# Performance work log

Measured on AMD Instinct MI355X. Metric: run time of the kernel, lower is better.

Reference implementation:

```python
import jax, jax.numpy as jnp
import numpy as np

B, T, C, H = 8, 1024, 768, 12  # GPT-2 small attention, block_size=1024

def setup_inputs() -> dict:
    key = jax.random.key(0)
    k0, k1, k2 = jax.random.split(key, 3)
    return {
        "x": jax.random.normal(k0, (1, B, T, C), jnp.float32) * 0.02,
        "w_attn": jax.random.normal(k1, (C, 3 * C), jnp.float32) * 0.02,
        "b_attn": jnp.zeros((3 * C,), jnp.float32),
        "w_proj": jax.random.normal(k2, (C, C), jnp.float32) * 0.02,
        "b_proj": jnp.zeros((C,), jnp.float32),
    }

def reference(x, w_attn, b_attn, w_proj, b_proj):
    _, b, t, c = x.shape
    d = c // H  # head dim
    xb = x[0]  # [B,T,C]
    qkv = xb @ w_attn + b_attn  # [B,T,3C]
    q, k, v = jnp.split(qkv, 3, axis=-1)
    def to_heads(u):
        return u.reshape(b, t, H, d).transpose(0, 2, 1, 3)  # [B,H,T,D]
    q, k, v = to_heads(q), to_heads(k), to_heads(v)
    scale = 1.0 / jnp.sqrt(jnp.asarray(d, q.dtype))
    att = jnp.einsum('bhqd,bhkd->bhqk', q, k) * scale  # [B,H,T,T]
    causal = jnp.tril(jnp.ones((t, t), bool))
    att = jnp.where(causal, att, -jnp.inf)
    att = jax.nn.softmax(att, axis=-1)
    y = jnp.einsum('bhqk,bhkd->bhqd', att, v)  # [B,H,T,D]
    y = y.transpose(0, 2, 1, 3).reshape(1, b, t, c)
    return y @ w_proj + b_proj
```

## Files before the change

### kernel.cpp

```cpp
#include <hip/hip_runtime.h>
#include <hip/hip_bf16.h>
#include <math.h>

#define Bq 8
#define Tq 1024
#define Cq 768
#define Hq 12
#define Dq 64
#define MROWS (Bq*Tq)
#define N_QKV (3*Cq)

typedef __bf16 bf16;
typedef bf16 bf16x8 __attribute__((ext_vector_type(8)));
typedef bf16 bf16x4 __attribute__((ext_vector_type(4)));
typedef float f32x4 __attribute__((ext_vector_type(4)));
typedef float f32x16 __attribute__((ext_vector_type(16)));
typedef unsigned int u32x4 __attribute__((ext_vector_type(4)));

#define MFMA16x16x32(a, b, c) __builtin_amdgcn_mfma_f32_16x16x32_bf16((a), (b), (c), 0, 0, 0)
#define MFMA32x32x16(a, b, c) __builtin_amdgcn_mfma_f32_32x32x16_bf16((a), (b), (c), 0, 0, 0)

__device__ __forceinline__ bf16x8& lds_v8(bf16* base, int row, int byteoff) {
    return *reinterpret_cast<bf16x8*>(
        reinterpret_cast<char*>(base) + row * 128 + (byteoff ^ ((row & 7) << 4)));
}

typedef __attribute__((address_space(3))) unsigned int lds_u32;
typedef const __attribute__((address_space(1))) unsigned int glb_u32;
__device__ __forceinline__ void gload16(const void* g, void* lds) {
    __builtin_amdgcn_global_load_lds((glb_u32*)(uintptr_t)g,
                                     (lds_u32*)(unsigned int)(uintptr_t)lds,
                                     16, 0, 0);
}

__device__ __forceinline__ unsigned cvtpk_bf16(float lo, float hi) {
    unsigned r;
    asm volatile("v_cvt_pk_bf16_f32 %0, %1, %2" : "=v"(r) : "v"(lo), "v"(hi));
    return r;
}

#define NA_CONV 3072
#define NB_WA   432
#define NB_WP   144
__global__ __launch_bounds__(256) void prep(const float* __restrict__ x,
                                            const float* __restrict__ wa,
                                            const float* __restrict__ wp,
                                            bf16* __restrict__ Ax,
                                            bf16* __restrict__ WaT,
                                            bf16* __restrict__ WpT) {
    __shared__ float tile[64][65];
    const int bid = blockIdx.x;
    if (bid < NA_CONV) {
        const int i = bid * 256 + threadIdx.x;
        const float4* p = reinterpret_cast<const float4*>(x) + (size_t)i * 2;
        float4 a = p[0], b = p[1];
        bf16x8 o;
        o[0] = (bf16)a.x; o[1] = (bf16)a.y; o[2] = (bf16)a.z; o[3] = (bf16)a.w;
        o[4] = (bf16)b.x; o[5] = (bf16)b.y; o[6] = (bf16)b.z; o[7] = (bf16)b.w;
        reinterpret_cast<bf16x8*>(Ax)[i] = o;
        return;
    }
    const float* src;
    bf16* dst;
    int C, tb, bxT;
    if (bid < NA_CONV + NB_WA) { tb = bid - NA_CONV; src = wa; dst = WaT; C = N_QKV; bxT = 36; }
    else                       { tb = bid - NA_CONV - NB_WA; src = wp; dst = WpT; C = Cq; bxT = 12; }
    const int R = Cq;
    const int bx = (tb % bxT) * 64, by = (tb / bxT) * 64;
    const int tx = threadIdx.x & 63, ty = threadIdx.x >> 6;
    #pragma unroll
    for (int i = 0; i < 64; i += 4)
        tile[ty + i][tx] = src[(size_t)(by + ty + i) * C + bx + tx];
    __syncthreads();
    #pragma unroll
    for (int i = 0; i < 64; i += 4)
        dst[(size_t)(bx + ty + i) * R + by + tx] = (bf16)tile[tx][ty + i];
}

__global__ __launch_bounds__(256) void gemm_qkv(const bf16* __restrict__ A,
                                                const bf16* __restrict__ Bt,
                                                const float* __restrict__ bias,
                                                bf16* __restrict__ Qo,
                                                bf16* __restrict__ Ko,
                                                bf16* __restrict__ Vto) {
    __shared__ bf16 As[2][128 * 64];
    __shared__ bf16 Bs[2][128 * 64];
    const int tid = threadIdx.x;
    const int w = tid >> 6, l = tid & 63;
    const int lane16 = l & 15, kg = l >> 4;
    const int wr = w >> 1, wc = w & 1;
    const int flat = blockIdx.x;
    const int nid = (flat & 7) * 144 + (flat >> 3);
    const int bn0 = (nid % 18) * 128, bm0 = (nid / 18) * 128;

    auto stage = [&](int k0, int buf) {
        #pragma unroll
        for (int j = 0; j < 4; ++j) {
            const int q8 = w * 4 + j;
            const int r  = q8 * 8 + (l >> 3);
            const int c16 = (l & 7) ^ (r & 7);
            gload16(A + (size_t)(bm0 + r) * Cq + k0 + c16 * 8, &As[buf][q8 * 512]);
            gload16(Bt + (size_t)(bn0 + r) * Cq + k0 + c16 * 8, &Bs[buf][q8 * 512]);
        }
    };

    f32x4 acc[4][4] = {};
    stage(0, 0);
    __syncthreads();
    for (int kt = 0; kt < 12; ++kt) {
        if (kt < 11) stage((kt + 1) * 64, (kt + 1) & 1);
        bf16* Ac = As[kt & 1];
        bf16* Bc = Bs[kt & 1];
        #pragma unroll
        for (int ks = 0; ks < 2; ++ks) {
            bf16x8 af[4], bfr[4];
            #pragma unroll
            for (int m = 0; m < 4; ++m)
                af[m] = lds_v8(Ac, wr * 64 + m * 16 + lane16, ks * 64 + kg * 16);
            #pragma unroll
            for (int n = 0; n < 4; ++n)
                bfr[n] = lds_v8(Bc, wc * 64 + n * 16 + lane16, ks * 64 + kg * 16);
            #pragma unroll
            for (int m = 0; m < 4; ++m)
                #pragma unroll
                for (int n = 0; n < 4; ++n)
                    acc[m][n] = MFMA16x16x32(af[m], bfr[n], acc[m][n]);
        }
        __syncthreads();
    }

    const int whichB = bn0 / Cq;
    char* Lt = (char*)&As[0][0];
    #pragma unroll
    for (int mi = 0; mi < 4; ++mi) {
        #pragma unroll
        for (int r = 0; r < 4; ++r) {
            const int m = wr * 64 + mi * 16 + kg * 4 + r;
            #pragma unroll
            for (int ni = 0; ni < 4; ++ni) {
                const int n = wc * 64 + ni * 16 + lane16;
                float v = acc[mi][ni][r] + bias[bn0 + n];
                if (whichB == 0) v *= 0.18033688011112042f;
                int a;
                if (whichB < 2) a = m * 256 + ((n * 2) ^ ((m & 7) << 4));
                else            a = n * 256 + ((m * 2) ^ ((n & 7) << 4));
                *reinterpret_cast<bf16*>(Lt + a) = (bf16)v;
            }
        }
    }
    __syncthreads();
    const int bb = bm0 >> 10, tt0 = bm0 & 1023;
    if (whichB < 2) {
        bf16* dst = whichB == 0 ? Qo : Ko;
        #pragma unroll
        for (int j = 0; j < 8; ++j) {
            const int c = j * 256 + tid;
            const int m = c >> 4, nc = c & 15;
            bf16x8 val = *reinterpret_cast<bf16x8*>(Lt + m * 256 + ((nc * 16) ^ ((m & 7) << 4)));
            const int gcol0 = bn0 + nc * 8;
            const int h = (gcol0 - whichB * Cq) >> 6;
            const int d0 = gcol0 & 63;
            *reinterpret_cast<bf16x8*>(dst + (((size_t)bb * Hq + h) * Tq + tt0 + m) * Dq + d0) = val;
        }
    } else {
        #pragma unroll
        for (int j = 0; j < 8; ++j) {
            const int c = j * 256 + tid;
            const int n = c >> 4, mc = c & 15;
            bf16x8 val = *reinterpret_cast<bf16x8*>(Lt + n * 256 + ((mc * 16) ^ ((n & 7) << 4)));
            const int gcol0 = bn0 + n;
            const int h = (gcol0 - 2 * Cq) >> 6;
            const int d = gcol0 & 63;
            *reinterpret_cast<bf16x8*>(Vto + (((size_t)bb * Hq + h) * Dq + d) * Tq + tt0 + mc * 8) = val;
        }
    }
}

__global__ __launch_bounds__(256) void attn_mfma(const bf16* __restrict__ Q,
                                                 const bf16* __restrict__ K,
                                                 const bf16* __restrict__ Vt,
                                                 bf16* __restrict__ Y) {
    const int tid = threadIdx.x;
    const int w = tid >> 6, l = tid & 63;
    const int l31 = l & 31, hi = l >> 5;
    const int b4 = blockIdx.x / 96;
    const int bh = blockIdx.x % 96;
    const int qt = 15 - (b4 * 4 + w);
    const size_t hoff = (size_t)bh * Tq * Dq;
    const int q0 = qt * 64;

    bf16x8 qf[2][4];
    #pragma unroll
    for (int sub = 0; sub < 2; ++sub)
        #pragma unroll
        for (int ds = 0; ds < 4; ++ds)
            qf[sub][ds] = *reinterpret_cast<const bf16x8*>(
                Q + hoff + (size_t)(q0 + sub * 32 + l31) * Dq + ds * 16 + hi * 8);

    f32x16 o[2][2] = {};
    float m_[2] = {-INFINITY, -INFINITY};
    float l_[2] = {0.f, 0.f};

    for (int t = 0; t <= qt; ++t) {
        const bf16* Kt  = K  + hoff + (size_t)(t * 64) * Dq;
        const bf16* Vtt = Vt + hoff + t * 64;
        bf16x8 kf[2][4];
        #pragma unroll
        for (int kh = 0; kh < 2; ++kh)
            #pragma unroll
            for (int ds = 0; ds < 4; ++ds)
                kf[kh][ds] = *reinterpret_cast<const bf16x8*>(
                    Kt + (size_t)(kh * 32 + l31) * Dq + ds * 16 + hi * 8);
        bf16x8 vf[4][2];
        #pragma unroll
        for (int ks = 0; ks < 4; ++ks)
            #pragma unroll
            for (int dh = 0; dh < 2; ++dh)
                vf[ks][dh] = *reinterpret_cast<const bf16x8*>(
                    Vtt + (size_t)(dh * 32 + l31) * Tq + ks * 16 + hi * 8);

        #pragma unroll
        for (int sub = 0; sub < 2; ++sub) {
            f32x16 s[2] = {};
            #pragma unroll
            for (int kh = 0; kh < 2; ++kh)
                #pragma unroll
                for (int ds = 0; ds < 4; ++ds)
                    s[kh] = MFMA32x32x16(kf[kh][ds], qf[sub][ds], s[kh]);
            if (t == qt) {
                #pragma unroll
                for (int kh = 0; kh < 2; ++kh)
                    #pragma unroll
                    for (int reg = 0; reg < 16; ++reg) {
                        const int kcol = (reg & 3) + 8 * (reg >> 2) + 4 * hi + kh * 32;
                        if (kcol > sub * 32 + l31) s[kh][reg] = -INFINITY;
                    }
            }
            float pmax = s[0][0];
            #pragma unroll
            for (int kh = 0; kh < 2; ++kh)
                #pragma unroll
                for (int reg = 0; reg < 16; ++reg) pmax = fmaxf(pmax, s[kh][reg]);
            pmax = fmaxf(pmax, __shfl_xor(pmax, 32));
            const float mn = fmaxf(m_[sub], pmax);
            const float alpha = exp2f(m_[sub] - mn);
            m_[sub] = mn;
            l_[sub] *= alpha;
            o[sub][0] *= alpha;
            o[sub][1] *= alpha;
            float lsum = 0.f;
            #pragma unroll
            for (int kh = 0; kh < 2; ++kh)
                #pragma unroll
                for (int reg = 0; reg < 16; ++reg) {
                    const float p = exp2f(s[kh][reg] - mn);
                    s[kh][reg] = p;
                    lsum += p;
                }
            l_[sub] += lsum;
            bf16x8 pa[4];
            #pragma unroll
            for (int kh = 0; kh < 2; ++kh)
                #pragma unroll
                for (int g = 0; g < 2; ++g) {
                    const int rb = g * 8;
                    const unsigned u01 = cvtpk_bf16(s[kh][rb + 0], s[kh][rb + 1]);
                    const unsigned u23 = cvtpk_bf16(s[kh][rb + 2], s[kh][rb + 3]);
                    const unsigned u45 = cvtpk_bf16(s[kh][rb + 4], s[kh][rb + 5]);
                    const unsigned u67 = cvtpk_bf16(s[kh][rb + 6], s[kh][rb + 7]);
                    const unsigned x01 = __shfl_xor(u01, 32);
                    const unsigned x23 = __shfl_xor(u23, 32);
                    const unsigned x45 = __shfl_xor(u45, 32);
                    const unsigned x67 = __shfl_xor(u67, 32);
                    u32x4 wv;
                    wv[0] = hi ? x45 : u01;
                    wv[1] = hi ? x67 : u23;
                    wv[2] = hi ? u45 : x01;
                    wv[3] = hi ? u67 : x23;
                    pa[kh * 2 + g] = __builtin_bit_cast(bf16x8, wv);
                }
            #pragma unroll
            for (int ks = 0; ks < 4; ++ks)
                #pragma unroll
                for (int dh = 0; dh < 2; ++dh)
                    o[sub][dh] = MFMA32x32x16(vf[ks][dh], pa[ks], o[sub][dh]);
        }
    }

    const int bb = bh / Hq, h = bh - bb * Hq;
    #pragma unroll
    for (int sub = 0; sub < 2; ++sub) {
        const float ltot = l_[sub] + __shfl_xor(l_[sub], 32);
        const float inv = 1.f / ltot;
        const int q = q0 + sub * 32 + l31;
        bf16* yp = Y + ((size_t)bb * Tq + q) * Cq + h * Dq;
        #pragma unroll
        for (int dh = 0; dh < 2; ++dh)
            #pragma unroll
            for (int rg = 0; rg < 4; ++rg) {
                const int d0 = 8 * rg + 4 * hi + 32 * dh;
                bf16x4 ov;
                #pragma unroll
                for (int j = 0; j < 4; ++j) ov[j] = (bf16)(o[sub][dh][rg * 4 + j] * inv);
                *reinterpret_cast<bf16x4*>(yp + d0) = ov;
            }
    }
}

__global__ __launch_bounds__(256) void gemm_proj(const bf16* __restrict__ A,
                                                 const bf16* __restrict__ Bt,
                                                 const float* __restrict__ bias,
                                                 float* __restrict__ out) {
    __shared__ bf16 As[2][128 * 64];
    __shared__ bf16 Bs[2][128 * 64];
    const int tid = threadIdx.x;
    const int w = tid >> 6, l = tid & 63;
    const int lane16 = l & 15, kg = l >> 4;
    const int wr = w >> 1, wc = w & 1;
    const int flat = blockIdx.x;
    const int nid = (flat & 7) * 48 + (flat >> 3);
    const int bn0 = (nid % 6) * 128, bm0 = (nid / 6) * 128;

    auto stage = [&](int k0, int buf) {
        #pragma unroll
        for (int j = 0; j < 4; ++j) {
            const int q8 = w * 4 + j;
            const int r  = q8 * 8 + (l >> 3);
            const int c16 = (l & 7) ^ (r & 7);
            gload16(A + (size_t)(bm0 + r) * Cq + k0 + c16 * 8, &As[buf][q8 * 512]);
            gload16(Bt + (size_t)(bn0 + r) * Cq + k0 + c16 * 8, &Bs[buf][q8 * 512]);
        }
    };

    f32x4 acc[4][4] = {};
    stage(0, 0);
    __syncthreads();
    for (int kt = 0; kt < 12; ++kt) {
        if (kt < 11) stage((kt + 1) * 64, (kt + 1) & 1);
        bf16* Ac = As[kt & 1];
        bf16* Bc = Bs[kt & 1];
        #pragma unroll
        for (int ks = 0; ks < 2; ++ks) {
            bf16x8 af[4], bfr[4];
            #pragma unroll
            for (int m = 0; m < 4; ++m)
                af[m] = lds_v8(Ac, wr * 64 + m * 16 + lane16, ks * 64 + kg * 16);
            #pragma unroll
            for (int n = 0; n < 4; ++n)
                bfr[n] = lds_v8(Bc, wc * 64 + n * 16 + lane16, ks * 64 + kg * 16);
            #pragma unroll
            for (int m = 0; m < 4; ++m)
                #pragma unroll
                for (int n = 0; n < 4; ++n)
                    acc[m][n] = MFMA16x16x32(af[m], bfr[n], acc[m][n]);
        }
        __syncthreads();
    }

    char* L32 = (char*)&As[0][0];
    #pragma unroll
    for (int half = 0; half < 2; ++half) {
        if (wc == half) {
            #pragma unroll
            for (int mi = 0; mi < 4; ++mi)
                #pragma unroll
                for (int r = 0; r < 4; ++r) {
                    const int m = wr * 64 + mi * 16 + kg * 4 + r;
                    #pragma unroll
                    for (int ni = 0; ni < 4; ++ni) {
                        const int nl = ni * 16 + lane16;
                        const float v = acc[mi][ni][r] + bias[bn0 + half * 64 + nl];
                        *reinterpret_cast<float*>(L32 + m * 256 + ((nl * 4) ^ ((m & 7) << 4))) = v;
                    }
                }
        }
        __syncthreads();
        #pragma unroll
        for (int j = 0; j < 8; ++j) {
            const int c = j * 256 + tid;
            const int m = c >> 4, nc = c & 15;
            float4 val = *reinterpret_cast<float4*>(L32 + m * 256 + ((nc * 16) ^ ((m & 7) << 4)));
            *reinterpret_cast<float4*>(out + (size_t)(bm0 + m) * Cq + bn0 + half * 64 + nc * 4) = val;
        }
        __syncthreads();
    }
}

extern "C" void kernel_launch(void* const* d_in, const int* in_sizes, int n_in,
                              void* d_out, int out_size, void* d_ws, size_t ws_size,
                              hipStream_t stream) {
    const float* x      = (const float*)d_in[0];
    const float* w_attn = (const float*)d_in[1];
    const float* b_attn = (const float*)d_in[2];
    const float* w_proj = (const float*)d_in[3];
    const float* b_proj = (const float*)d_in[4];
    float* out = (float*)d_out;

    char* ws = (char*)d_ws;
    bf16* Ax  = (bf16*)ws; ws += (size_t)MROWS * Cq * 2;
    bf16* WaT = (bf16*)ws; ws += (size_t)N_QKV * Cq * 2;
    bf16* WpT = (bf16*)ws; ws += (size_t)Cq * Cq * 2;
    bf16* Qw  = (bf16*)ws; ws += (size_t)MROWS * Cq * 2;
    bf16* Kw  = (bf16*)ws; ws += (size_t)MROWS * Cq * 2;
    bf16* Vtw = (bf16*)ws; ws += (size_t)MROWS * Cq * 2;
    bf16* Yw  = (bf16*)ws; ws += (size_t)MROWS * Cq * 2;

    prep<<<dim3(NA_CONV + NB_WA + NB_WP), 256, 0, stream>>>(x, w_attn, w_proj, Ax, WaT, WpT);
    gemm_qkv<<<dim3(1152), 256, 0, stream>>>(Ax, WaT, b_attn, Qw, Kw, Vtw);
    attn_mfma<<<dim3(384), 256, 0, stream>>>(Qw, Kw, Vtw, Yw);
    gemm_proj<<<dim3(384), 256, 0, stream>>>(Yw, WpT, b_proj, out);
}
```

Before: 116.3 us.

## Split attention into 32-row query strips per wave with half-tile diagonal skip

Each wave now handles one 32-row query strip instead of two, which doubles the grid to 768 blocks and shortens the critical path of the longest causal rows. On the diagonal tile, when the strip is the first half of a 64-key tile, the second K/V half is skipped entirely, removing fully masked MFMA work. It also adds a lazy rescale that only updates the running max and accumulator when some lane's new max exceeds the old one by more than 8 (in log2 units). The trade-off is that each loaded K/V tile is reused by half as many query rows, so K/V traffic from global memory or cache goes up.

```diff
diff --git a/kernel.cpp b/kernel.cpp
--- a/kernel.cpp
+++ b/kernel.cpp
@@ -183,128 +183,170 @@
     const int tid = threadIdx.x;
     const int w = tid >> 6, l = tid & 63;
     const int l31 = l & 31, hi = l >> 5;
-    const int b4 = blockIdx.x / 96;
+    const int g = blockIdx.x / 96;
     const int bh = blockIdx.x % 96;
-    const int qt = 15 - (b4 * 4 + w);
+    const int qs = 31 - (g * 4 + w);
+    const int q0 = qs * 32;
+    const int nt = (qs >> 1) + 1;
     const size_t hoff = (size_t)bh * Tq * Dq;
-    const int q0 = qt * 64;
-
-    bf16x8 qf[2][4];
-    #pragma unroll
-    for (int sub = 0; sub < 2; ++sub)
-        #pragma unroll
-        for (int ds = 0; ds < 4; ++ds)
-            qf[sub][ds] = *reinterpret_cast<const bf16x8*>(
-                Q + hoff + (size_t)(q0 + sub * 32 + l31) * Dq + ds * 16 + hi * 8);
-
-    f32x16 o[2][2] = {};
-    float m_[2] = {-INFINITY, -INFINITY};
-    float l_[2] = {0.f, 0.f};
-
-    for (int t = 0; t <= qt; ++t) {
+
+    bf16x8 qf[4];
+    #pragma unroll
+    for (int ds = 0; ds < 4; ++ds)
+        qf[ds] = *reinterpret_cast<const bf16x8*>(
+            Q + hoff + (size_t)(q0 + l31) * Dq + ds * 16 + hi * 8);
+
+    f32x16 o[2] = {};
+    float m_ = -INFINITY, l_ = 0.f;
+
+    for (int t = 0; t < nt; ++t) {
+        const bool diag = (t == nt - 1);
+        const bool half = diag && !(qs & 1);
         const bf16* Kt  = K  + hoff + (size_t)(t * 64) * Dq;
         const bf16* Vtt = Vt + hoff + t * 64;
-        bf16x8 kf[2][4];
-        #pragma unroll
-        for (int kh = 0; kh < 2; ++kh)
+
+        bf16x8 kf0[4], kf1[4];
+        #pragma unroll
+        for (int ds = 0; ds < 4; ++ds)
+            kf0[ds] = *reinterpret_cast<const bf16x8*>(
+                Kt + (size_t)l31 * Dq + ds * 16 + hi * 8);
+        if (!half) {
             #pragma unroll
             for (int ds = 0; ds < 4; ++ds)
-                kf[kh][ds] = *reinterpret_cast<const bf16x8*>(
-                    Kt + (size_t)(kh * 32 + l31) * Dq + ds * 16 + hi * 8);
+                kf1[ds] = *reinterpret_cast<const bf16x8*>(
+                    Kt + (size_t)(32 + l31) * Dq + ds * 16 + hi * 8);
+        }
         bf16x8 vf[4][2];
         #pragma unroll
-        for (int ks = 0; ks < 4; ++ks)
+        for (int ks = 0; ks < 2; ++ks)
             #pragma unroll
             for (int dh = 0; dh < 2; ++dh)
                 vf[ks][dh] = *reinterpret_cast<const bf16x8*>(
                     Vtt + (size_t)(dh * 32 + l31) * Tq + ks * 16 + hi * 8);
-
-        #pragma unroll
-        for (int sub = 0; sub < 2; ++sub) {
-            f32x16 s[2] = {};
-            #pragma unroll
-            for (int kh = 0; kh < 2; ++kh)
-                #pragma unroll
-                for (int ds = 0; ds < 4; ++ds)
-                    s[kh] = MFMA32x32x16(kf[kh][ds], qf[sub][ds], s[kh]);
-            if (t == qt) {
-                #pragma unroll
-                for (int kh = 0; kh < 2; ++kh)
-                    #pragma unroll
-                    for (int reg = 0; reg < 16; ++reg) {
-                        const int kcol = (reg & 3) + 8 * (reg >> 2) + 4 * hi + kh * 32;
-                        if (kcol > sub * 32 + l31) s[kh][reg] = -INFINITY;
-                    }
-            }
-            float pmax = s[0][0];
-            #pragma unroll
-            for (int kh = 0; kh < 2; ++kh)
-                #pragma unroll
-                for (int reg = 0; reg < 16; ++reg) pmax = fmaxf(pmax, s[kh][reg]);
-            pmax = fmaxf(pmax, __shfl_xor(pmax, 32));
-            const float mn = fmaxf(m_[sub], pmax);
-            const float alpha = exp2f(m_[sub] - mn);
-            m_[sub] = mn;
-            l_[sub] *= alpha;
-            o[sub][0] *= alpha;
-            o[sub][1] *= alpha;
-            float lsum = 0.f;
-            #pragma unroll
-            for (int kh = 0; kh < 2; ++kh)
-                #pragma unroll
-                for (int reg = 0; reg < 16; ++reg) {
-                    const float p = exp2f(s[kh][reg] - mn);
-                    s[kh][reg] = p;
-                    lsum += p;
-                }
-            l_[sub] += lsum;
-            bf16x8 pa[4];
-            #pragma unroll
-            for (int kh = 0; kh < 2; ++kh)
-                #pragma unroll
-                for (int g = 0; g < 2; ++g) {
-                    const int rb = g * 8;
-                    const unsigned u01 = cvtpk_bf16(s[kh][rb + 0], s[kh][rb + 1]);
-                    const unsigned u23 = cvtpk_bf16(s[kh][rb + 2], s[kh][rb + 3]);
-                    const unsigned u45 = cvtpk_bf16(s[kh][rb + 4], s[kh][rb + 5]);
-                    const unsigned u67 = cvtpk_bf16(s[kh][rb + 6], s[kh][rb + 7]);
-                    const unsigned x01 = __shfl_xor(u01, 32);
-                    const unsigned x23 = __shfl_xor(u23, 32);
-                    const unsigned x45 = __shfl_xor(u45, 32);
-                    const unsigned x67 = __shfl_xor(u67, 32);
-                    u32x4 wv;
-                    wv[0] = hi ? x45 : u01;
-                    wv[1] = hi ? x67 : u23;
-                    wv[2] = hi ? u45 : x01;
-                    wv[3] = hi ? u67 : x23;
-                    pa[kh * 2 + g] = __builtin_bit_cast(bf16x8, wv);
-                }
-            #pragma unroll
-            for (int ks = 0; ks < 4; ++ks)
+        if (!half) {
+            #pragma unroll
+            for (int ks = 2; ks < 4; ++ks)
                 #pragma unroll
                 for (int dh = 0; dh < 2; ++dh)
-                    o[sub][dh] = MFMA32x32x16(vf[ks][dh], pa[ks], o[sub][dh]);
+                    vf[ks][dh] = *reinterpret_cast<const bf16x8*>(
+                        Vtt + (size_t)(dh * 32 + l31) * Tq + ks * 16 + hi * 8);
+        }
+
+        f32x16 s0 = {}, s1 = {};
+        #pragma unroll
+        for (int ds = 0; ds < 4; ++ds) s0 = MFMA32x32x16(kf0[ds], qf[ds], s0);
+        if (!half) {
+            #pragma unroll
+            for (int ds = 0; ds < 4; ++ds) s1 = MFMA32x32x16(kf1[ds], qf[ds], s1);
+        }
+        if (diag) {
+            #pragma unroll
+            for (int reg = 0; reg < 16; ++reg) {
+                const int kg_ = t * 64 + (reg & 3) + 8 * (reg >> 2) + 4 * hi;
+                if (kg_ > q0 + l31) s0[reg] = -INFINITY;
+                if (!half && kg_ + 32 > q0 + l31) s1[reg] = -INFINITY;
+            }
+        }
+        float pmax = -INFINITY;
+        #pragma unroll
+        for (int reg = 0; reg < 16; ++reg) pmax = fmaxf(pmax, s0[reg]);
+        if (!half) {
+            #pragma unroll
+            for (int reg = 0; reg < 16; ++reg) pmax = fmaxf(pmax, s1[reg]);
+        }
+        pmax = fmaxf(pmax, __shfl_xor(pmax, 32));
+        if (!__all(pmax <= m_ + 8.f)) {
+            const float mn = fmaxf(m_, pmax);
+            const float alpha = exp2f(m_ - mn);
+            m_ = mn;
+            l_ *= alpha;
+            o[0] *= alpha;
+            o[1] *= alpha;
+        }
+        float lsum = 0.f;
+        #pragma unroll
+        for (int reg = 0; reg < 16; ++reg) {
+            const float p = exp2f(s0[reg] - m_);
+            s0[reg] = p;
+            lsum += p;
+        }
+        if (!half) {
+            #pragma unroll
+            for (int reg = 0; reg < 16; ++reg) {
+                const float p = exp2f(s1[reg] - m_);
+                s1[reg] = p;
+                lsum += p;
+            }
+        }
+        l_ += lsum;
+
+        bf16x8 pa[4];
+        #pragma unroll
+        for (int g2 = 0; g2 < 2; ++g2) {
+            const int rb = g2 * 8;
+            const unsigned u01 = cvtpk_bf16(s0[rb + 0], s0[rb + 1]);
+            const unsigned u23 = cvtpk_bf16(s0[rb + 2], s0[rb + 3]);
+            const unsigned u45 = cvtpk_bf16(s0[rb + 4], s0[rb + 5]);
+            const unsigned u67 = cvtpk_bf16(s0[rb + 6], s0[rb + 7]);
+            const unsigned x01 = __shfl_xor(u01, 32);
+            const unsigned x23 = __shfl_xor(u23, 32);
+            const unsigned x45 = __shfl_xor(u45, 32);
+            const unsigned x67 = __shfl_xor(u67, 32);
+            u32x4 wv;
+            wv[0] = hi ? x45 : u01;
+            wv[1] = hi ? x67 : u23;
+            wv[2] = hi ? u45 : x01;
+            wv[3] = hi ? u67 : x23;
+            pa[g2] = __builtin_bit_cast(bf16x8, wv);
+        }
+        if (!half) {
+            #pragma unroll
+            for (int g2 = 0; g2 < 2; ++g2) {
+                const int rb = g2 * 8;
+                const unsigned u01 = cvtpk_bf16(s1[rb + 0], s1[rb + 1]);
+                const unsigned u23 = cvtpk_bf16(s1[rb + 2], s1[rb + 3]);
+                const unsigned u45 = cvtpk_bf16(s1[rb + 4], s1[rb + 5]);
+                const unsigned u67 = cvtpk_bf16(s1[rb + 6], s1[rb + 7]);
+                const unsigned x01 = __shfl_xor(u01, 32);
+                const unsigned x23 = __shfl_xor(u23, 32);
+                const unsigned x45 = __shfl_xor(u45, 32);
+                const unsigned x67 = __shfl_xor(u67, 32);
+                u32x4 wv;
+                wv[0] = hi ? x45 : u01;
+                wv[1] = hi ? x67 : u23;
+                wv[2] = hi ? u45 : x01;
+                wv[3] = hi ? u67 : x23;
+                pa[2 + g2] = __builtin_bit_cast(bf16x8, wv);
+            }
+        }
+        #pragma unroll
+        for (int ks = 0; ks < 2; ++ks)
+            #pragma unroll
+            for (int dh = 0; dh < 2; ++dh)
+                o[dh] = MFMA32x32x16(vf[ks][dh], pa[ks], o[dh]);
+        if (!half) {
+            #pragma unroll
+            for (int ks = 2; ks < 4; ++ks)
+                #pragma unroll
+                for (int dh = 0; dh < 2; ++dh)
+                    o[dh] = MFMA32x32x16(vf[ks][dh], pa[ks], o[dh]);
         }
     }
 
     const int bb = bh / Hq, h = bh - bb * Hq;
-    #pragma unroll
-    for (int sub = 0; sub < 2; ++sub) {
-        const float ltot = l_[sub] + __shfl_xor(l_[sub], 32);
-        const float inv = 1.f / ltot;
-        const int q = q0 + sub * 32 + l31;
-        bf16* yp = Y + ((size_t)bb * Tq + q) * Cq + h * Dq;
-        #pragma unroll
-        for (int dh = 0; dh < 2; ++dh)
-            #pragma unroll
-            for (int rg = 0; rg < 4; ++rg) {
-                const int d0 = 8 * rg + 4 * hi + 32 * dh;
-                bf16x4 ov;
-                #pragma unroll
-                for (int j = 0; j < 4; ++j) ov[j] = (bf16)(o[sub][dh][rg * 4 + j] * inv);
-                *reinterpret_cast<bf16x4*>(yp + d0) = ov;
-            }
-    }
+    const float ltot = l_ + __shfl_xor(l_, 32);
+    const float inv = 1.f / ltot;
+    bf16* yp = Y + ((size_t)bb * Tq + q0 + l31) * Cq + h * Dq;
+    #pragma unroll
+    for (int dh = 0; dh < 2; ++dh)
+        #pragma unroll
+        for (int rg = 0; rg < 4; ++rg) {
+            const int d0 = 8 * rg + 4 * hi + 32 * dh;
+            bf16x4 ov;
+            #pragma unroll
+            for (int j = 0; j < 4; ++j) ov[j] = (bf16)(o[dh][rg * 4 + j] * inv);
+            *reinterpret_cast<bf16x4*>(yp + d0) = ov;
+        }
 }
 
 __global__ __launch_bounds__(256) void gemm_proj(const bf16* __restrict__ A,
@@ -407,6 +449,6 @@
 
     prep<<<dim3(NA_CONV + NB_WA + NB_WP), 256, 0, stream>>>(x, w_attn, w_proj, Ax, WaT, WpT);
     gemm_qkv<<<dim3(1152), 256, 0, stream>>>(Ax, WaT, b_attn, Qw, Kw, Vtw);
-    attn_mfma<<<dim3(384), 256, 0, stream>>>(Qw, Kw, Vtw, Yw);
+    attn_mfma<<<dim3(768), 256, 0, stream>>>(Qw, Kw, Vtw, Yw);
     gemm_proj<<<dim3(384), 256, 0, stream>>>(Yw, WpT, b_proj, out);
 }
```

New measurement: 125.0 us. +7.5%, slower.

## Split attention KV range across wave pairs and balance causal tiles per block

Applied to the files above, without the earlier changes.

Each query tile is now handled by two waves that split its KV loop in half, and their partial softmax states are merged through shared memory. Each block pairs a long tile with a short one (qt and 15-qt), and the grid doubles to 768 blocks, mapped so that heads stay grouped per XCD. The diagonal tile also skips the fully masked upper-half MFMAs, and the max rescale runs only when the running max grows by more than a threshold. The change adds LDS use, a block barrier and merge work in exchange for better load balance and occupancy.

```diff
diff --git a/kernel.cpp b/kernel.cpp
--- a/kernel.cpp
+++ b/kernel.cpp
@@ -180,12 +180,21 @@
                                                  const bf16* __restrict__ K,
                                                  const bf16* __restrict__ Vt,
                                                  bf16* __restrict__ Y) {
+    __shared__ float OlS[2][4][16][64];
+    __shared__ float MLs[2][2][2][64];
     const int tid = threadIdx.x;
     const int w = tid >> 6, l = tid & 63;
     const int l31 = l & 31, hi = l >> 5;
-    const int b4 = blockIdx.x / 96;
-    const int bh = blockIdx.x % 96;
-    const int qt = 15 - (b4 * 4 + w);
+    const int pair = w >> 1, s = w & 1;
+    const int id = blockIdx.x;
+    const int xcd = id & 7, j = id >> 3;
+    const int bh = xcd * 12 + (j >> 3);
+    const int jj = j & 7;
+    const int qt = pair == 0 ? (15 - jj) : jj;
+    const int n = qt + 1;
+    const int half0 = (n + 1) >> 1;
+    const int t0 = s == 0 ? 0 : half0;
+    const int t1 = s == 0 ? half0 : n;
     const size_t hoff = (size_t)bh * Tq * Dq;
     const int q0 = qt * 64;
 
@@ -201,7 +210,7 @@
     float m_[2] = {-INFINITY, -INFINITY};
     float l_[2] = {0.f, 0.f};
 
-    for (int t = 0; t <= qt; ++t) {
+    for (int t = t0; t < t1; ++t) {
         const bf16* Kt  = K  + hoff + (size_t)(t * 64) * Dq;
         const bf16* Vtt = Vt + hoff + t * 64;
         bf16x8 kf[2][4];
@@ -218,56 +227,70 @@
             for (int dh = 0; dh < 2; ++dh)
                 vf[ks][dh] = *reinterpret_cast<const bf16x8*>(
                     Vtt + (size_t)(dh * 32 + l31) * Tq + ks * 16 + hi * 8);
+        const bool diag = (t == qt);
 
         #pragma unroll
         for (int sub = 0; sub < 2; ++sub) {
-            f32x16 s[2] = {};
-            #pragma unroll
-            for (int kh = 0; kh < 2; ++kh)
-                #pragma unroll
-                for (int ds = 0; ds < 4; ++ds)
-                    s[kh] = MFMA32x32x16(kf[kh][ds], qf[sub][ds], s[kh]);
-            if (t == qt) {
-                #pragma unroll
-                for (int kh = 0; kh < 2; ++kh)
-                    #pragma unroll
-                    for (int reg = 0; reg < 16; ++reg) {
-                        const int kcol = (reg & 3) + 8 * (reg >> 2) + 4 * hi + kh * 32;
-                        if (kcol > sub * 32 + l31) s[kh][reg] = -INFINITY;
-                    }
-            }
-            float pmax = s[0][0];
-            #pragma unroll
-            for (int kh = 0; kh < 2; ++kh)
-                #pragma unroll
-                for (int reg = 0; reg < 16; ++reg) pmax = fmaxf(pmax, s[kh][reg]);
+            const bool skipHi = diag && (sub == 0);
+            f32x16 sv[2] = {};
+            #pragma unroll
+            for (int ds = 0; ds < 4; ++ds) sv[0] = MFMA32x32x16(kf[0][ds], qf[sub][ds], sv[0]);
+            if (!skipHi) {
+                #pragma unroll
+                for (int ds = 0; ds < 4; ++ds) sv[1] = MFMA32x32x16(kf[1][ds], qf[sub][ds], sv[1]);
+            }
+            if (diag) {
+                #pragma unroll
+                for (int reg = 0; reg < 16; ++reg) {
+                    const int kcol = (reg & 3) + 8 * (reg >> 2) + 4 * hi;
+                    if (kcol > sub * 32 + l31) sv[0][reg] = -INFINITY;
+                    if (!skipHi && kcol + 32 > sub * 32 + l31) sv[1][reg] = -INFINITY;
+                }
+            }
+            float pmax = -INFINITY;
+            #pragma unroll
+            for (int reg = 0; reg < 16; ++reg) pmax = fmaxf(pmax, sv[0][reg]);
+            if (!skipHi) {
+                #pragma unroll
+                for (int reg = 0; reg < 16; ++reg) pmax = fmaxf(pmax, sv[1][reg]);
+            }
             pmax = fmaxf(pmax, __shfl_xor(pmax, 32));
-            const float mn = fmaxf(m_[sub], pmax);
-            const float alpha = exp2f(m_[sub] - mn);
-            m_[sub] = mn;
-            l_[sub] *= alpha;
-            o[sub][0] *= alpha;
-            o[sub][1] *= alpha;
+            if (!__all(pmax <= m_[sub] + 8.f)) {
+                const float mn = fmaxf(m_[sub], pmax);
+                const float alpha = exp2f(m_[sub] - mn);
+                m_[sub] = mn;
+                l_[sub] *= alpha;
+                o[sub][0] *= alpha;
+                o[sub][1] *= alpha;
+            }
             float lsum = 0.f;
             #pragma unroll
-            for (int kh = 0; kh < 2; ++kh)
+            for (int reg = 0; reg < 16; ++reg) {
+                const float p = exp2f(sv[0][reg] - m_[sub]);
+                sv[0][reg] = p;
+                lsum += p;
+            }
+            if (!skipHi) {
                 #pragma unroll
                 for (int reg = 0; reg < 16; ++reg) {
-                    const float p = exp2f(s[kh][reg] - mn);
-                    s[kh][reg] = p;
+                    const float p = exp2f(sv[1][reg] - m_[sub]);
+                    sv[1][reg] = p;
                     lsum += p;
                 }
+            }
             l_[sub] += lsum;
+
             bf16x8 pa[4];
             #pragma unroll
-            for (int kh = 0; kh < 2; ++kh)
-                #pragma unroll
-                for (int g = 0; g < 2; ++g) {
-                    const int rb = g * 8;
-                    const unsigned u01 = cvtpk_bf16(s[kh][rb + 0], s[kh][rb + 1]);
-                    const unsigned u23 = cvtpk_bf16(s[kh][rb + 2], s[kh][rb + 3]);
-                    const unsigned u45 = cvtpk_bf16(s[kh][rb + 4], s[kh][rb + 5]);
-                    const unsigned u67 = cvtpk_bf16(s[kh][rb + 6], s[kh][rb + 7]);
+            for (int kh = 0; kh < 2; ++kh) {
+                if (kh == 1 && skipHi) break;
+                #pragma unroll
+                for (int g2 = 0; g2 < 2; ++g2) {
+                    const int rb = g2 * 8;
+                    const unsigned u01 = cvtpk_bf16(sv[kh][rb + 0], sv[kh][rb + 1]);
+                    const unsigned u23 = cvtpk_bf16(sv[kh][rb + 2], sv[kh][rb + 3]);
+                    const unsigned u45 = cvtpk_bf16(sv[kh][rb + 4], sv[kh][rb + 5]);
+                    const unsigned u67 = cvtpk_bf16(sv[kh][rb + 6], sv[kh][rb + 7]);
                     const unsigned x01 = __shfl_xor(u01, 32);
                     const unsigned x23 = __shfl_xor(u23, 32);
                     const unsigned x45 = __shfl_xor(u45, 32);
@@ -277,33 +300,67 @@
                     wv[1] = hi ? x67 : u23;
                     wv[2] = hi ? u45 : x01;
                     wv[3] = hi ? u67 : x23;
-                    pa[kh * 2 + g] = __builtin_bit_cast(bf16x8, wv);
+                    pa[kh * 2 + g2] = __builtin_bit_cast(bf16x8, wv);
                 }
-            #pragma unroll
-            for (int ks = 0; ks < 4; ++ks)
+            }
+            #pragma unroll
+            for (int ks = 0; ks < 2; ++ks)
                 #pragma unroll
                 for (int dh = 0; dh < 2; ++dh)
                     o[sub][dh] = MFMA32x32x16(vf[ks][dh], pa[ks], o[sub][dh]);
-        }
-    }
-
-    const int bb = bh / Hq, h = bh - bb * Hq;
-    #pragma unroll
-    for (int sub = 0; sub < 2; ++sub) {
-        const float ltot = l_[sub] + __shfl_xor(l_[sub], 32);
-        const float inv = 1.f / ltot;
-        const int q = q0 + sub * 32 + l31;
-        bf16* yp = Y + ((size_t)bb * Tq + q) * Cq + h * Dq;
-        #pragma unroll
-        for (int dh = 0; dh < 2; ++dh)
-            #pragma unroll
-            for (int rg = 0; rg < 4; ++rg) {
-                const int d0 = 8 * rg + 4 * hi + 32 * dh;
-                bf16x4 ov;
-                #pragma unroll
-                for (int j = 0; j < 4; ++j) ov[j] = (bf16)(o[sub][dh][rg * 4 + j] * inv);
-                *reinterpret_cast<bf16x4*>(yp + d0) = ov;
-            }
+            if (!skipHi) {
+                #pragma unroll
+                for (int ks = 2; ks < 4; ++ks)
+                    #pragma unroll
+                    for (int dh = 0; dh < 2; ++dh)
+                        o[sub][dh] = MFMA32x32x16(vf[ks][dh], pa[ks], o[sub][dh]);
+            }
+        }
+    }
+
+    if (s == 1) {
+        #pragma unroll
+        for (int sub = 0; sub < 2; ++sub) {
+            MLs[pair][0][sub][l] = m_[sub];
+            MLs[pair][1][sub][l] = l_[sub];
+            #pragma unroll
+            for (int dh = 0; dh < 2; ++dh)
+                #pragma unroll
+                for (int reg = 0; reg < 16; ++reg)
+                    OlS[pair][sub * 2 + dh][reg][l] = o[sub][dh][reg];
+        }
+    }
+    __syncthreads();
+    if (s == 0) {
+        const int bb = bh / Hq, h = bh - bb * Hq;
+        #pragma unroll
+        for (int sub = 0; sub < 2; ++sub) {
+            const float m1 = MLs[pair][0][sub][l];
+            const float l1 = MLs[pair][1][sub][l];
+            const float mn = fmaxf(m_[sub], m1);
+            const float a0 = exp2f(m_[sub] - mn);
+            const float a1 = exp2f(m1 - mn);
+            float lm = l_[sub] * a0 + l1 * a1;
+            const float ltot = lm + __shfl_xor(lm, 32);
+            const float inv = 1.f / ltot;
+            const int q = q0 + sub * 32 + l31;
+            bf16* yp = Y + ((size_t)bb * Tq + q) * Cq + h * Dq;
+            #pragma unroll
+            for (int dh = 0; dh < 2; ++dh) {
+                f32x16 om;
+                #pragma unroll
+                for (int reg = 0; reg < 16; ++reg)
+                    om[reg] = o[sub][dh][reg] * a0 + OlS[pair][sub * 2 + dh][reg][l] * a1;
+                #pragma unroll
+                for (int rg = 0; rg < 4; ++rg) {
+                    const int d0 = 8 * rg + 4 * hi + 32 * dh;
+                    bf16x4 ov;
+                    #pragma unroll
+                    for (int jx = 0; jx < 4; ++jx) ov[jx] = (bf16)(om[rg * 4 + jx] * inv);
+                    *reinterpret_cast<bf16x4*>(yp + d0) = ov;
+                }
+            }
+        }
     }
 }
 
@@ -407,6 +464,6 @@
 
     prep<<<dim3(NA_CONV + NB_WA + NB_WP), 256, 0, stream>>>(x, w_attn, w_proj, Ax, WaT, WpT);
     gemm_qkv<<<dim3(1152), 256, 0, stream>>>(Ax, WaT, b_attn, Qw, Kw, Vtw);
-    attn_mfma<<<dim3(384), 256, 0, stream>>>(Qw, Kw, Vtw, Yw);
+    attn_mfma<<<dim3(768), 256, 0, stream>>>(Qw, Kw, Vtw, Yw);
     gemm_proj<<<dim3(384), 256, 0, stream>>>(Yw, WpT, b_proj, out);
 }
```

Measured after the change: 145.5 us. +25.1%, slower.

## Store K and V in 8-element chunked layouts for coalesced attention fragment loads

Applied to the files above, without the earlier changes.

The QKV GEMM epilogue now writes K as [bh][d/8][T][8] and V as [bh][T/8][D][8], replacing row-major K and transposed V. The attention kernel's per-lane 16-byte fragment loads then become contiguous across the 32 lanes, so each wave's global loads cover fewer cache lines. The trade-off is more scattered stores in the GEMM epilogue and a non-standard intermediate layout that both kernels must agree on.

```diff
diff --git a/kernel.cpp b/kernel.cpp
--- a/kernel.cpp
+++ b/kernel.cpp
@@ -81,8 +81,8 @@
                                                 const bf16* __restrict__ Bt,
                                                 const float* __restrict__ bias,
                                                 bf16* __restrict__ Qo,
-                                                bf16* __restrict__ Ko,
-                                                bf16* __restrict__ Vto) {
+                                                bf16* __restrict__ K8,
+                                                bf16* __restrict__ V8) {
     __shared__ bf16 As[2][128 * 64];
     __shared__ bf16 Bs[2][128 * 64];
     const int tid = threadIdx.x;
@@ -150,35 +150,47 @@
     }
     __syncthreads();
     const int bb = bm0 >> 10, tt0 = bm0 & 1023;
-    if (whichB < 2) {
-        bf16* dst = whichB == 0 ? Qo : Ko;
+    if (whichB == 0) {
         #pragma unroll
         for (int j = 0; j < 8; ++j) {
             const int c = j * 256 + tid;
             const int m = c >> 4, nc = c & 15;
             bf16x8 val = *reinterpret_cast<bf16x8*>(Lt + m * 256 + ((nc * 16) ^ ((m & 7) << 4)));
             const int gcol0 = bn0 + nc * 8;
-            const int h = (gcol0 - whichB * Cq) >> 6;
+            const int h = gcol0 >> 6;
             const int d0 = gcol0 & 63;
-            *reinterpret_cast<bf16x8*>(dst + (((size_t)bb * Hq + h) * Tq + tt0 + m) * Dq + d0) = val;
-        }
-    } else {
+            *reinterpret_cast<bf16x8*>(Qo + (((size_t)bb * Hq + h) * Tq + tt0 + m) * Dq + d0) = val;
+        }
+    } else if (whichB == 1) {
         #pragma unroll
         for (int j = 0; j < 8; ++j) {
             const int c = j * 256 + tid;
-            const int n = c >> 4, mc = c & 15;
+            const int m = c & 127, nc = c >> 7;
+            bf16x8 val = *reinterpret_cast<bf16x8*>(Lt + m * 256 + ((nc * 16) ^ ((m & 7) << 4)));
+            const int hn = bn0 + nc * 8 - Cq;
+            const int h = hn >> 6, d8 = (hn >> 3) & 7;
+            *reinterpret_cast<bf16x8*>(
+                K8 + ((((size_t)bb * Hq + h) * 8 + d8) * Tq + tt0 + m) * 8) = val;
+        }
+    } else {
+        #pragma unroll
+        for (int j = 0; j < 8; ++j) {
+            const int c = j * 256 + tid;
+            const int d6 = c & 63, rest = c >> 6;
+            const int hh = rest & 1, mc = rest >> 1;
+            const int n = hh * 64 + d6;
             bf16x8 val = *reinterpret_cast<bf16x8*>(Lt + n * 256 + ((mc * 16) ^ ((n & 7) << 4)));
-            const int gcol0 = bn0 + n;
-            const int h = (gcol0 - 2 * Cq) >> 6;
-            const int d = gcol0 & 63;
-            *reinterpret_cast<bf16x8*>(Vto + (((size_t)bb * Hq + h) * Dq + d) * Tq + tt0 + mc * 8) = val;
+            const int hn = bn0 + n - 2 * Cq;
+            const int h = hn >> 6, d = hn & 63;
+            *reinterpret_cast<bf16x8*>(
+                V8 + ((((size_t)bb * Hq + h) * 128 + (tt0 >> 3) + mc) * Dq + d) * 8) = val;
         }
     }
 }
 
 __global__ __launch_bounds__(256) void attn_mfma(const bf16* __restrict__ Q,
-                                                 const bf16* __restrict__ K,
-                                                 const bf16* __restrict__ Vt,
+                                                 const bf16* __restrict__ K8,
+                                                 const bf16* __restrict__ V8,
                                                  bf16* __restrict__ Y) {
     const int tid = threadIdx.x;
     const int w = tid >> 6, l = tid & 63;
@@ -187,6 +199,7 @@
     const int bh = blockIdx.x % 96;
     const int qt = 15 - (b4 * 4 + w);
     const size_t hoff = (size_t)bh * Tq * Dq;
+    const size_t base8 = (size_t)bh * (Tq * Dq);
     const int q0 = qt * 64;
 
     bf16x8 qf[2][4];
@@ -202,22 +215,20 @@
     float l_[2] = {0.f, 0.f};
 
     for (int t = 0; t <= qt; ++t) {
-        const bf16* Kt  = K  + hoff + (size_t)(t * 64) * Dq;
-        const bf16* Vtt = Vt + hoff + t * 64;
         bf16x8 kf[2][4];
         #pragma unroll
         for (int kh = 0; kh < 2; ++kh)
             #pragma unroll
             for (int ds = 0; ds < 4; ++ds)
                 kf[kh][ds] = *reinterpret_cast<const bf16x8*>(
-                    Kt + (size_t)(kh * 32 + l31) * Dq + ds * 16 + hi * 8);
+                    K8 + base8 + ((size_t)(ds * 2 + hi) * Tq + t * 64 + kh * 32 + l31) * 8);
         bf16x8 vf[4][2];
         #pragma unroll
         for (int ks = 0; ks < 4; ++ks)
             #pragma unroll
             for (int dh = 0; dh < 2; ++dh)
                 vf[ks][dh] = *reinterpret_cast<const bf16x8*>(
-                    Vtt + (size_t)(dh * 32 + l31) * Tq + ks * 16 + hi * 8);
+                    V8 + base8 + ((size_t)(t * 8 + ks * 2 + hi) * Dq + dh * 32 + l31) * 8);
 
         #pragma unroll
         for (int sub = 0; sub < 2; ++sub) {
@@ -401,12 +412,12 @@
     bf16* WaT = (bf16*)ws; ws += (size_t)N_QKV * Cq * 2;
     bf16* WpT = (bf16*)ws; ws += (size_t)Cq * Cq * 2;
     bf16* Qw  = (bf16*)ws; ws += (size_t)MROWS * Cq * 2;
-    bf16* Kw  = (bf16*)ws; ws += (size_t)MROWS * Cq * 2;
-    bf16* Vtw = (bf16*)ws; ws += (size_t)MROWS * Cq * 2;
+    bf16* K8w = (bf16*)ws; ws += (size_t)MROWS * Cq * 2;
+    bf16* V8w = (bf16*)ws; ws += (size_t)MROWS * Cq * 2;
     bf16* Yw  = (bf16*)ws; ws += (size_t)MROWS * Cq * 2;
 
     prep<<<dim3(NA_CONV + NB_WA + NB_WP), 256, 0, stream>>>(x, w_attn, w_proj, Ax, WaT, WpT);
-    gemm_qkv<<<dim3(1152), 256, 0, stream>>>(Ax, WaT, b_attn, Qw, Kw, Vtw);
-    attn_mfma<<<dim3(384), 256, 0, stream>>>(Qw, Kw, Vtw, Yw);
+    gemm_qkv<<<dim3(1152), 256, 0, stream>>>(Ax, WaT, b_attn, Qw, K8w, V8w);
+    attn_mfma<<<dim3(384), 256, 0, stream>>>(Qw, K8w, V8w, Yw);
     gemm_proj<<<dim3(384), 256, 0, stream>>>(Yw, WpT, b_proj, out);
 }
```

Result: no change. 114.6 us (-1.5%).
